# Kernel tuning notes

Measured on AMD Instinct MI355X. Metric: run time of the kernel, lower is better.

The kernel has to match this reference:

```python
import jax, jax.numpy as jnp
import numpy as np

# dims (see shape_source)
B, U, W, N, H = 4, 32, 128, 8, 64
MODEL_DIMS = N * H            # 512, must equal N*H
LEFT_CONTEXT = 128
l = LEFT_CONTEXT - 1          # 127
r = 0
C = W + l + r                 # 255 = context_size
F = l + r + 1                 # 128 relative positions
MAX_TIMESCALE = 10000.0


def _timing_signal_1d_pos(position, channels):
    """Sinusoidal embeddings for explicit positions. position: (1, F)."""
    position = position.astype(jnp.float32)
    num_timescales = channels // 2
    log_inc = jnp.log(MAX_TIMESCALE) / max(num_timescales - 1, 1)
    inv_timescales = jnp.exp(jnp.arange(num_timescales, dtype=jnp.float32) * -log_inc)
    scaled_time = position[:, :, None] * inv_timescales[None, None, :]
    sig = jnp.concatenate([jnp.sin(scaled_time), jnp.cos(scaled_time)], axis=2)
    # channels is even here, so no pad needed (original pads channels % 2)
    return sig  # (1, F, channels), float32


def setup_inputs():
    key = jax.random.key(0)
    k1, k2, k3 = jax.random.split(key, 3)
    queries = jax.random.normal(k1, (B, U, W, N, H), dtype=jnp.float32)
    keys = jax.random.normal(k2, (B, U, C, N, H), dtype=jnp.float32)
    # glorot_uniform for DenseGeneral kernel (model_dims,) -> (N, H)
    limit = float(np.sqrt(6.0 / (MODEL_DIMS + N * H)))
    pos_kernel = jax.random.uniform(k3, (MODEL_DIMS, N, H), jnp.float32, -limit, limit)
    return {"queries": queries, "keys": keys, "pos_kernel": pos_kernel}


def reference(queries, keys, pos_kernel):
    # Term AC: content-based logits  (B, N, U, W, C)
    term_ac = jnp.einsum('BuwNH,BucNH->BNuwc', queries, keys, precision='highest')

    # Relative positions l, l-1, ..., 0  (shape (1, F))
    pos = jnp.arange(l, -r - 1, -1)[None, :]
    sin_emb = _timing_signal_1d_pos(pos, MODEL_DIMS)          # (1, F, D)
    sin_emb = jnp.einsum('xFD,DNH->xFNH', sin_emb, pos_kernel)[0]  # (F, N, H)

    # Term BD: query @ relative-position embedding  (B, N, U, W, F)
    term_bd = jnp.einsum('BuwNH,FNH->BNuwF', queries, sin_emb, precision='highest')

    # Relative shift trick: pad last dim to C+1, flatten, slice, reshape to (.., W, C)
    term_bd = jnp.pad(term_bd, ((0, 0), (0, 0), (0, 0), (0, 0), (0, C + 1 - F)))
    term_bd = term_bd.reshape(B, N, U, W * (C + 1))[:, :, :, :W * C]
    term_bd = term_bd.reshape(B, N, U, W, C)

    return term_ac + term_bd
```

## Files before the change

kernel.cpp:

```cpp
#include <hip/hip_runtime.h>
#include <hip/hip_bf16.h>


typedef __bf16 bf16x8 __attribute__((ext_vector_type(8)));
typedef float f32x4 __attribute__((ext_vector_type(4)));

#define MFMA16(a, b, c) __builtin_amdgcn_mfma_f32_16x16x32_bf16((a), (b), (c), 0, 0, 0)

__device__ __forceinline__ unsigned short f2bf(float x) {
  unsigned u = __float_as_uint(x);
  u += 0x7FFFu + ((u >> 16) & 1u);
  return (unsigned short)(u >> 16);
}

__global__ __launch_bounds__(512) void compute_E(const float* __restrict__ pk,
                                                 unsigned short* __restrict__ E) {
  const int f = blockIdx.x;
  const int t = threadIdx.x;
  __shared__ float sv[256], cv[256];
  if (t < 256) {
    const float L = 9.210340371976184f / 255.0f;
    float ang = (float)(127 - f) * expf(-L * (float)t);
    sv[t] = sinf(ang);
    cv[t] = cosf(ang);
  }
  __syncthreads();
  float acc = 0.f;
#pragma unroll 8
  for (int i = 0; i < 256; ++i)
    acc = fmaf(sv[i], pk[i * 512 + t], fmaf(cv[i], pk[(i + 256) * 512 + t], acc));
  const int n = t >> 6, h = t & 63;
  E[(n * 128 + f) * 64 + h] = f2bf(acc);
}

__global__ __launch_bounds__(512) void txl_main(const float* __restrict__ Q,
                                                const float* __restrict__ K,
                                                const unsigned short* __restrict__ E,
                                                float* __restrict__ out) {
  __shared__ unsigned short Qs[128 * 72];
  __shared__ unsigned short Ks[256 * 72];
  __shared__ unsigned short Es[128 * 72];
  __shared__ float bds[128 * 129];

  const int tid = threadIdx.x;
  const int blk = blockIdx.x;
  const int n  = blk & 7;
  const int bu = blk >> 3;

  const float* gq = Q + (size_t)bu * (128 * 512) + n * 64;
#pragma unroll
  for (int i = 0; i < 4; ++i) {
    int fi = i * 512 + tid;
    int row = fi >> 4, c4 = fi & 15;
    float4 v = *(const float4*)(gq + row * 512 + c4 * 4);
    ushort4 r;
    r.x = f2bf(v.x); r.y = f2bf(v.y); r.z = f2bf(v.z); r.w = f2bf(v.w);
    *(ushort4*)(&Qs[row * 72 + c4 * 4]) = r;
  }
  const float* gk = K + (size_t)bu * (255 * 512) + n * 64;
#pragma unroll
  for (int i = 0; i < 8; ++i) {
    int fi = i * 512 + tid;
    int row = fi >> 4, c4 = fi & 15;
    float4 v;
    if (row < 255) v = *(const float4*)(gk + row * 512 + c4 * 4);
    else { v.x = 0.f; v.y = 0.f; v.z = 0.f; v.w = 0.f; }
    ushort4 r;
    r.x = f2bf(v.x); r.y = f2bf(v.y); r.z = f2bf(v.z); r.w = f2bf(v.w);
    *(ushort4*)(&Ks[row * 72 + c4 * 4]) = r;
  }
#pragma unroll
  for (int i = 0; i < 2; ++i) {
    int t2 = i * 512 + tid;
    uint4 v = *((const uint4*)(E + n * (128 * 64)) + t2);
    *(uint4*)(&Es[(t2 >> 3) * 72 + (t2 & 7) * 8]) = v;
  }
  __syncthreads();

  const int l = tid & 63, wv = tid >> 6;
  const int a = l & 15, g = l >> 4;

  {
    const int r0 = wv * 16;
    const int arow = (r0 + a) * 72 + g * 8;
    bf16x8 qa0 = *(const bf16x8*)&Qs[arow];
    bf16x8 qa1 = *(const bf16x8*)&Qs[arow + 32];
#pragma unroll
    for (int ft = 0; ft < 8; ++ft) {
      const int f0 = ft * 16;
      const int brow = (f0 + a) * 72 + g * 8;
      bf16x8 eb0 = *(const bf16x8*)&Es[brow];
      bf16x8 eb1 = *(const bf16x8*)&Es[brow + 32];
      f32x4 acc = {0.f, 0.f, 0.f, 0.f};
      acc = MFMA16(qa0, eb0, acc);
      acc = MFMA16(qa1, eb1, acc);
      const int wrow = r0 + g * 4;
#pragma unroll
      for (int j = 0; j < 4; ++j)
        bds[(wrow + j) * 129 + f0 + a] = acc[j];
    }
  }
  __syncthreads();

  const int b = bu >> 5, u = bu & 31;
  float* gout = out + (size_t)((b * 8 + n) * 32 + u) * (128 * 255);
#pragma unroll
  for (int rt = 0; rt < 8; ++rt) {
    const int r0 = rt * 16;
    const int arow = (r0 + a) * 72 + g * 8;
    bf16x8 qa0 = *(const bf16x8*)&Qs[arow];
    bf16x8 qa1 = *(const bf16x8*)&Qs[arow + 32];
#pragma unroll
    for (int ct = 0; ct < 2; ++ct) {
      const int c0 = wv * 32 + ct * 16;
      const int brow = (c0 + a) * 72 + g * 8;
      bf16x8 kb0 = *(const bf16x8*)&Ks[brow];
      bf16x8 kb1 = *(const bf16x8*)&Ks[brow + 32];
      f32x4 acc = {0.f, 0.f, 0.f, 0.f};
      acc = MFMA16(qa0, kb0, acc);
      acc = MFMA16(qa1, kb1, acc);
      const int c = c0 + a;
#pragma unroll
      for (int j = 0; j < 4; ++j) {
        const int row = r0 + g * 4 + j;
        const int f = c - row;
        float val = acc[j];
        if ((unsigned)f < 128u) val += bds[row * 129 + f];
        if (c < 255) gout[(size_t)row * 255 + c] = val;
      }
    }
  }
}

extern "C" void kernel_launch(void* const* d_in, const int* in_sizes, int n_in,
                              void* d_out, int out_size, void* d_ws, size_t ws_size,
                              hipStream_t stream) {
  const float* q  = (const float*)d_in[0];
  const float* k  = (const float*)d_in[1];
  const float* pk = (const float*)d_in[2];
  float* out = (float*)d_out;
  unsigned short* E = (unsigned short*)d_ws;

  compute_E<<<dim3(128), dim3(512), 0, stream>>>(pk, E);
  txl_main<<<dim3(1024), dim3(512), 0, stream>>>(q, k, E, out);
}
```

Measured before the change: 247.8 us.

## Split context dimension across blocks and shrink LDS to raise occupancy

The main kernel now uses a 2D grid that splits the 255-wide context into two 128-column halves, so each block holds only 128 key rows. Key loads are prefetched into registers and reuse the shared buffer that held the position embeddings, and the BD term is stored as bf16 in LDS. A launch bound of 4 blocks per CU is requested. compute_E is split into 256 blocks of 256 threads. Together these cut LDS per block to raise occupancy and parallelism, at the cost of recomputing the BD term and reloading Q in both halves, plus extra rounding of BD to bf16.

```diff
diff --git a/kernel.cpp b/kernel.cpp
--- a/kernel.cpp
+++ b/kernel.cpp
@@ -12,13 +12,17 @@
   u += 0x7FFFu + ((u >> 16) & 1u);
   return (unsigned short)(u >> 16);
 }
+__device__ __forceinline__ float bf2f(unsigned short x) {
+  return __uint_as_float((unsigned)x << 16);
+}
 
-__global__ __launch_bounds__(512) void compute_E(const float* __restrict__ pk,
+__global__ __launch_bounds__(256) void compute_E(const float* __restrict__ pk,
                                                  unsigned short* __restrict__ E) {
-  const int f = blockIdx.x;
+  const int f = blockIdx.x >> 1, half = blockIdx.x & 1;
   const int t = threadIdx.x;
+  const int nh = half * 256 + t;
   __shared__ float sv[256], cv[256];
-  if (t < 256) {
+  {
     const float L = 9.210340371976184f / 255.0f;
     float ang = (float)(127 - f) * expf(-L * (float)t);
     sv[t] = sinf(ang);
@@ -28,24 +32,23 @@
   float acc = 0.f;
 #pragma unroll 8
   for (int i = 0; i < 256; ++i)
-    acc = fmaf(sv[i], pk[i * 512 + t], fmaf(cv[i], pk[(i + 256) * 512 + t], acc));
-  const int n = t >> 6, h = t & 63;
+    acc = fmaf(sv[i], pk[i * 512 + nh], fmaf(cv[i], pk[(i + 256) * 512 + nh], acc));
+  const int n = nh >> 6, h = nh & 63;
   E[(n * 128 + f) * 64 + h] = f2bf(acc);
 }
 
-__global__ __launch_bounds__(512) void txl_main(const float* __restrict__ Q,
-                                                const float* __restrict__ K,
-                                                const unsigned short* __restrict__ E,
-                                                float* __restrict__ out) {
+__global__ __launch_bounds__(512, 4) void txl_main(const float* __restrict__ Q,
+                                                   const float* __restrict__ K,
+                                                   const unsigned short* __restrict__ E,
+                                                   float* __restrict__ out) {
   __shared__ unsigned short Qs[128 * 72];
-  __shared__ unsigned short Ks[256 * 72];
-  __shared__ unsigned short Es[128 * 72];
-  __shared__ float bds[128 * 129];
+  __shared__ unsigned short Un[128 * 72];
+  __shared__ unsigned short bds[128 * 130];
 
   const int tid = threadIdx.x;
-  const int blk = blockIdx.x;
-  const int n  = blk & 7;
-  const int bu = blk >> 3;
+  const int n  = blockIdx.x & 7;
+  const int bu = blockIdx.x >> 3;
+  const int c0base = (int)blockIdx.y * 128;
 
   const float* gq = Q + (size_t)bu * (128 * 512) + n * 64;
 #pragma unroll
@@ -57,77 +60,77 @@
     r.x = f2bf(v.x); r.y = f2bf(v.y); r.z = f2bf(v.z); r.w = f2bf(v.w);
     *(ushort4*)(&Qs[row * 72 + c4 * 4]) = r;
   }
-  const float* gk = K + (size_t)bu * (255 * 512) + n * 64;
-#pragma unroll
-  for (int i = 0; i < 8; ++i) {
-    int fi = i * 512 + tid;
-    int row = fi >> 4, c4 = fi & 15;
-    float4 v;
-    if (row < 255) v = *(const float4*)(gk + row * 512 + c4 * 4);
-    else { v.x = 0.f; v.y = 0.f; v.z = 0.f; v.w = 0.f; }
-    ushort4 r;
-    r.x = f2bf(v.x); r.y = f2bf(v.y); r.z = f2bf(v.z); r.w = f2bf(v.w);
-    *(ushort4*)(&Ks[row * 72 + c4 * 4]) = r;
-  }
 #pragma unroll
   for (int i = 0; i < 2; ++i) {
     int t2 = i * 512 + tid;
     uint4 v = *((const uint4*)(E + n * (128 * 64)) + t2);
-    *(uint4*)(&Es[(t2 >> 3) * 72 + (t2 & 7) * 8]) = v;
+    *(uint4*)(&Un[(t2 >> 3) * 72 + (t2 & 7) * 8]) = v;
+  }
+  const float* gk = K + (size_t)bu * (255 * 512) + n * 64;
+  float4 kr[4];
+#pragma unroll
+  for (int i = 0; i < 4; ++i) {
+    int fi = i * 512 + tid;
+    int r = fi >> 4, c4 = fi & 15;
+    int c = c0base + r;
+    if (c < 255) kr[i] = *(const float4*)(gk + (size_t)c * 512 + c4 * 4);
+    else { kr[i].x = 0.f; kr[i].y = 0.f; kr[i].z = 0.f; kr[i].w = 0.f; }
   }
   __syncthreads();
 
   const int l = tid & 63, wv = tid >> 6;
   const int a = l & 15, g = l >> 4;
+  const int r0 = wv * 16;
+  const int arow = (r0 + a) * 72 + g * 8;
+  bf16x8 qa0 = *(const bf16x8*)&Qs[arow];
+  bf16x8 qa1 = *(const bf16x8*)&Qs[arow + 32];
 
-  {
-    const int r0 = wv * 16;
-    const int arow = (r0 + a) * 72 + g * 8;
-    bf16x8 qa0 = *(const bf16x8*)&Qs[arow];
-    bf16x8 qa1 = *(const bf16x8*)&Qs[arow + 32];
 #pragma unroll
-    for (int ft = 0; ft < 8; ++ft) {
-      const int f0 = ft * 16;
-      const int brow = (f0 + a) * 72 + g * 8;
-      bf16x8 eb0 = *(const bf16x8*)&Es[brow];
-      bf16x8 eb1 = *(const bf16x8*)&Es[brow + 32];
-      f32x4 acc = {0.f, 0.f, 0.f, 0.f};
-      acc = MFMA16(qa0, eb0, acc);
-      acc = MFMA16(qa1, eb1, acc);
-      const int wrow = r0 + g * 4;
+  for (int ft = 0; ft < 8; ++ft) {
+    const int f0 = ft * 16;
+    const int brow = (f0 + a) * 72 + g * 8;
+    bf16x8 eb0 = *(const bf16x8*)&Un[brow];
+    bf16x8 eb1 = *(const bf16x8*)&Un[brow + 32];
+    f32x4 acc = {0.f, 0.f, 0.f, 0.f};
+    acc = MFMA16(qa0, eb0, acc);
+    acc = MFMA16(qa1, eb1, acc);
+    const int wrow = r0 + g * 4;
 #pragma unroll
-      for (int j = 0; j < 4; ++j)
-        bds[(wrow + j) * 129 + f0 + a] = acc[j];
-    }
+    for (int j = 0; j < 4; ++j)
+      bds[(wrow + j) * 130 + f0 + a] = f2bf(acc[j]);
+  }
+  __syncthreads();
+
+#pragma unroll
+  for (int i = 0; i < 4; ++i) {
+    int fi = i * 512 + tid;
+    int r = fi >> 4, c4 = fi & 15;
+    ushort4 rr;
+    rr.x = f2bf(kr[i].x); rr.y = f2bf(kr[i].y);
+    rr.z = f2bf(kr[i].z); rr.w = f2bf(kr[i].w);
+    *(ushort4*)(&Un[r * 72 + c4 * 4]) = rr;
   }
   __syncthreads();
 
   const int b = bu >> 5, u = bu & 31;
   float* gout = out + (size_t)((b * 8 + n) * 32 + u) * (128 * 255);
 #pragma unroll
-  for (int rt = 0; rt < 8; ++rt) {
-    const int r0 = rt * 16;
-    const int arow = (r0 + a) * 72 + g * 8;
-    bf16x8 qa0 = *(const bf16x8*)&Qs[arow];
-    bf16x8 qa1 = *(const bf16x8*)&Qs[arow + 32];
+  for (int ct = 0; ct < 8; ++ct) {
+    const int cc0 = ct * 16;
+    const int brow = (cc0 + a) * 72 + g * 8;
+    bf16x8 kb0 = *(const bf16x8*)&Un[brow];
+    bf16x8 kb1 = *(const bf16x8*)&Un[brow + 32];
+    f32x4 acc = {0.f, 0.f, 0.f, 0.f};
+    acc = MFMA16(qa0, kb0, acc);
+    acc = MFMA16(qa1, kb1, acc);
+    const int c = c0base + cc0 + a;
 #pragma unroll
-    for (int ct = 0; ct < 2; ++ct) {
-      const int c0 = wv * 32 + ct * 16;
-      const int brow = (c0 + a) * 72 + g * 8;
-      bf16x8 kb0 = *(const bf16x8*)&Ks[brow];
-      bf16x8 kb1 = *(const bf16x8*)&Ks[brow + 32];
-      f32x4 acc = {0.f, 0.f, 0.f, 0.f};
-      acc = MFMA16(qa0, kb0, acc);
-      acc = MFMA16(qa1, kb1, acc);
-      const int c = c0 + a;
-#pragma unroll
-      for (int j = 0; j < 4; ++j) {
-        const int row = r0 + g * 4 + j;
-        const int f = c - row;
-        float val = acc[j];
-        if ((unsigned)f < 128u) val += bds[row * 129 + f];
-        if (c < 255) gout[(size_t)row * 255 + c] = val;
-      }
+    for (int j = 0; j < 4; ++j) {
+      const int row = r0 + g * 4 + j;
+      const int f = c - row;
+      float val = acc[j];
+      if ((unsigned)f < 128u) val += bf2f(bds[row * 130 + f]);
+      if (c < 255) gout[(size_t)row * 255 + c] = val;
     }
   }
 }
@@ -141,6 +144,6 @@
   float* out = (float*)d_out;
   unsigned short* E = (unsigned short*)d_ws;
 
-  compute_E<<<dim3(128), dim3(512), 0, stream>>>(pk, E);
-  txl_main<<<dim3(1024), dim3(512), 0, stream>>>(q, k, E, out);
+  compute_E<<<dim3(256), dim3(256), 0, stream>>>(pk, E);
+  txl_main<<<dim3(1024, 2), dim3(512), 0, stream>>>(q, k, E, out);
 }
```

After: 366.1 us. +47.7%, slower.
